# Kernel optimization log

Measured on AMD Instinct MI355X. Metric: run time of the kernel, lower is better.

## Reference

```python
import jax, jax.numpy as jnp
import numpy as np

D_MODEL = 1024
NUM_HEADS = 16
DEPTH = D_MODEL // NUM_HEADS  # 64
BATCH = 2
SEQ = 2048


def setup_inputs() -> dict:
    key = jax.random.key(0)
    ks = jax.random.split(key, 11)
    s = 0.02
    return {
        "q": jax.random.normal(ks[0], (BATCH, SEQ, D_MODEL), dtype=jnp.float32),
        "k": jax.random.normal(ks[1], (BATCH, SEQ, D_MODEL), dtype=jnp.float32),
        "v": jax.random.normal(ks[2], (BATCH, SEQ, D_MODEL), dtype=jnp.float32),
        "wq": jax.random.normal(ks[3], (D_MODEL, D_MODEL), dtype=jnp.float32) * s,
        "bq": jnp.zeros((D_MODEL,), dtype=jnp.float32),
        "wk": jax.random.normal(ks[4], (D_MODEL, D_MODEL), dtype=jnp.float32) * s,
        "bk": jnp.zeros((D_MODEL,), dtype=jnp.float32),
        "wv": jax.random.normal(ks[5], (D_MODEL, D_MODEL), dtype=jnp.float32) * s,
        "bv": jnp.zeros((D_MODEL,), dtype=jnp.float32),
        "wo": jax.random.normal(ks[6], (D_MODEL, D_MODEL), dtype=jnp.float32) * s,
        "bo": jnp.zeros((D_MODEL,), dtype=jnp.float32),
    }


def reference(q, k, v, wq, bq, wk, bk, wv, bv, wo, bo):
    B = q.shape[0]
    # QKV projections, then split heads: (B, S, H, D)
    qh = (q @ wq + bq).reshape(B, -1, NUM_HEADS, DEPTH)
    kh = (k @ wk + bk).reshape(B, -1, NUM_HEADS, DEPTH)
    vh = (v @ wv + bv).reshape(B, -1, NUM_HEADS, DEPTH)

    inv_sqrt_dk = 1.0 / jnp.sqrt(jnp.float32(DEPTH))
    # scores: (B, Lq, Lk, H)
    scores = jnp.einsum('blhd,bjhd->bljh', qh, kh) * inv_sqrt_dk
    attn = jax.nn.softmax(scores, axis=2)
    # NOTE: original code divides by sqrt(dk) a SECOND time after softmax (faithful quirk)
    attn = attn * inv_sqrt_dk
    out = jnp.einsum('bljh,bjhe->blhe', attn, vh).reshape(B, -1, NUM_HEADS * DEPTH)
    return out @ wo + bo
```

## Files before the change

### kernel.cpp

```cpp
#include <hip/hip_runtime.h>
#include <math.h>

#define D_MODEL 1024
#define NHEADS 16
#define DH 64
#define BATCH 2
#define SEQ 2048
#define M_TOTAL (BATCH * SEQ)

typedef __attribute__((ext_vector_type(8))) short bf16x8;
typedef __attribute__((ext_vector_type(4))) float f32x4;
typedef __attribute__((ext_vector_type(16))) float f32x16;
typedef __attribute__((ext_vector_type(8))) unsigned short ushort8;
typedef unsigned short u16;
typedef unsigned int u32;

#define SCALE_Q 0.18033688f

static __device__ __forceinline__ u16 f2bf(float x) {
  unsigned int u = __float_as_uint(x);
  unsigned int r = (u + 0x7fffu + ((u >> 16) & 1u)) >> 16;
  return (u16)r;
}
static __device__ __forceinline__ u32 pk2bf(float a, float b) {
  return (u32)f2bf(a) | ((u32)f2bf(b) << 16);
}
static __device__ __forceinline__ u32 pkhu(float a, float b) {
  return __builtin_amdgcn_perm(__float_as_uint(b) + 0x8000u,
                               __float_as_uint(a) + 0x8000u, 0x07060302u);
}
static __device__ __forceinline__ float exp2fast(float x) {
  return __builtin_amdgcn_exp2f(x);
}

static __device__ __forceinline__ void gl_lds16(const u16* g, u16* l) {
  __builtin_amdgcn_global_load_lds(
      (const __attribute__((address_space(1))) u32*)g,
      (__attribute__((address_space(3))) u32*)l, 16, 0, 0);
}

__global__ __launch_bounds__(256) void prep_kernel(
    const float* __restrict__ q, const float* __restrict__ k, const float* __restrict__ v,
    u16* __restrict__ qb, u16* __restrict__ kb, u16* __restrict__ vb,
    const float* __restrict__ w0, const float* __restrict__ w1,
    const float* __restrict__ w2, const float* __restrict__ w3,
    u16* __restrict__ t0, u16* __restrict__ t1,
    u16* __restrict__ t2, u16* __restrict__ t3) {
  __shared__ float tf[64 * 68];
  const int z = blockIdx.z;
  const int tid = threadIdx.x;
  if (z < 3) {
    const float* src = (z == 0) ? q : (z == 1) ? k : v;
    u16* dst = (z == 0) ? qb : (z == 1) ? kb : vb;
    const size_t i = ((size_t)blockIdx.x * 256 + tid) * 8;
    float4 a = *reinterpret_cast<const float4*>(src + i);
    float4 b = *reinterpret_cast<const float4*>(src + i + 4);
    u32 o0 = pk2bf(a.x, a.y), o1 = pk2bf(a.z, a.w);
    u32 o2 = pk2bf(b.x, b.y), o3 = pk2bf(b.z, b.w);
    *reinterpret_cast<uint4*>(dst + i) = make_uint4(o0, o1, o2, o3);
    return;
  }
  if (blockIdx.x >= 256) return;
  const int zz = z - 3;
  const float* w = (zz == 0) ? w0 : (zz == 1) ? w1 : (zz == 2) ? w2 : w3;
  u16* wt = (zz == 0) ? t0 : (zz == 1) ? t1 : (zz == 2) ? t2 : t3;
  const int n0 = (blockIdx.x & 15) * 64, k0 = (blockIdx.x >> 4) * 64;
  const int kl = tid >> 4, nq = (tid & 15) * 4;
#pragma unroll
  for (int c = 0; c < 4; ++c) {
    float4 vv = *reinterpret_cast<const float4*>(
        &w[(size_t)(k0 + kl + c * 16) * 1024 + n0 + nq]);
    *reinterpret_cast<float4*>(&tf[(kl + c * 16) * 68 + nq]) = vv;
  }
  __syncthreads();
  const int n = tid & 63, kq = tid >> 6;
  u32 pk[8];
#pragma unroll
  for (int p = 0; p < 8; ++p) {
    float a = tf[(kq * 16 + 2 * p) * 68 + n];
    float b = tf[(kq * 16 + 2 * p + 1) * 68 + n];
    pk[p] = pk2bf(a, b);
  }
  u16* dst = &wt[(size_t)(n0 + n) * 1024 + k0 + kq * 16];
  *reinterpret_cast<uint4*>(dst) = make_uint4(pk[0], pk[1], pk[2], pk[3]);
  *reinterpret_cast<uint4*>(dst + 8) = make_uint4(pk[4], pk[5], pk[6], pk[7]);
}

__global__ __launch_bounds__(256) void qkv_gemm_kernel(
    const u16* __restrict__ qb, const u16* __restrict__ kb, const u16* __restrict__ vb,
    const u16* __restrict__ wqT, const u16* __restrict__ wkT, const u16* __restrict__ wvT,
    const float* __restrict__ bq, const float* __restrict__ bk, const float* __restrict__ bv,
    u16* __restrict__ qh, u16* __restrict__ kh, u16* __restrict__ vhT) {
  __shared__ u16 lds[16384];

  const int z = blockIdx.z;
  const u16* A  = (z == 0) ? qb : (z == 1) ? kb : vb;
  const u16* BT = (z == 0) ? wqT : (z == 1) ? wkT : wvT;
  const float* bias = (z == 0) ? bq : (z == 1) ? bk : bv;

  int wg = blockIdx.x + 8 * blockIdx.y;
  wg = (wg & 7) * 32 + (wg >> 3);
  const int m0 = (wg >> 3) * 128;
  const int n0 = (wg & 7) * 128;

  const int tid = threadIdx.x;
  const int w = tid >> 6, l = tid & 63;
  const int wr = w >> 1, wc = w & 1;
  const int n = l & 15, g = l >> 4;

  const u16* Ab = A + (size_t)(m0 + w * 16 + (l >> 2)) * 1024 + (l & 3) * 8;
  const u16* Bb = BT + (size_t)(n0 + w * 16 + (l >> 2)) * 1024 + (l & 3) * 8;
  const int wb = w * 512;

  f32x4 acc[4][4];
#pragma unroll
  for (int fm = 0; fm < 4; ++fm)
#pragma unroll
    for (int fn = 0; fn < 4; ++fn) acc[fm][fn] = (f32x4)(0.0f);

  gl_lds16(Ab, lds + wb);
  gl_lds16(Ab + (size_t)64 * 1024, lds + wb + 2048);
  gl_lds16(Bb, lds + 8192 + wb);
  gl_lds16(Bb + (size_t)64 * 1024, lds + 8192 + wb + 2048);
  __syncthreads();

  int cur = 0;
  for (int kk = 0; kk < 1024; kk += 32) {
    u16* sAc = lds + cur * 4096;
    u16* sBc = lds + 8192 + cur * 4096;
    if (kk + 32 < 1024) {
      u16* sAn = lds + (cur ^ 1) * 4096;
      u16* sBn = lds + 8192 + (cur ^ 1) * 4096;
      gl_lds16(Ab + kk + 32, sAn + wb);
      gl_lds16(Ab + kk + 32 + (size_t)64 * 1024, sAn + wb + 2048);
      gl_lds16(Bb + kk + 32, sBn + wb);
      gl_lds16(Bb + kk + 32 + (size_t)64 * 1024, sBn + wb + 2048);
    }
    bf16x8 af[4], bf[4];
#pragma unroll
    for (int f = 0; f < 4; ++f)
      af[f] = *reinterpret_cast<const bf16x8*>(&sAc[(wr * 64 + f * 16 + n) * 32 + g * 8]);
#pragma unroll
    for (int f = 0; f < 4; ++f)
      bf[f] = *reinterpret_cast<const bf16x8*>(&sBc[(wc * 64 + f * 16 + n) * 32 + g * 8]);
#pragma unroll
    for (int fm = 0; fm < 4; ++fm)
#pragma unroll
      for (int fn = 0; fn < 4; ++fn)
        acc[fm][fn] = __builtin_amdgcn_mfma_f32_16x16x32_bf16(af[fm], bf[fn], acc[fm][fn], 0, 0, 0);
    __syncthreads();
    cur ^= 1;
  }

  float bv4[4];
#pragma unroll
  for (int fn = 0; fn < 4; ++fn) bv4[fn] = bias[n0 + wc * 64 + fn * 16 + n];

  if (z < 2) {
    const float scale = (z == 0) ? SCALE_Q : 1.0f;
    u16* dst = (z == 0) ? qh : kh;
#pragma unroll
    for (int fm = 0; fm < 4; ++fm)
#pragma unroll
      for (int fn = 0; fn < 4; ++fn)
#pragma unroll
        for (int rr = 0; rr < 4; ++rr) {
          const int row = m0 + wr * 64 + fm * 16 + g * 4 + rr;
          const int col = n0 + wc * 64 + fn * 16 + n;
          dst[(size_t)row * 1024 + col] = f2bf((acc[fm][fn][rr] + bv4[fn]) * scale);
        }
  } else {
    __syncthreads();
    u16* bw = lds + w * 2304;
    const int hh = (n0 >> 6) + wc;
    const int bb = m0 >> 11;
    const int c = l >> 1, half = l & 1;
    const int sbase = (m0 & 2047) + wr * 64 + half * 32;
#pragma unroll
    for (int p = 0; p < 2; ++p) {
#pragma unroll
      for (int fh = 0; fh < 2; ++fh) {
        const int fn = p * 2 + fh;
#pragma unroll
        for (int fm = 0; fm < 4; ++fm)
#pragma unroll
          for (int rr = 0; rr < 4; ++rr)
            bw[(fh * 16 + n) * 72 + fm * 16 + g * 4 + rr] =
                f2bf(acc[fm][fn][rr] + bv4[fn]);
      }
      __syncthreads();
      u16* gd = vhT + ((size_t)((bb * NHEADS + hh) * DH + p * 32 + c)) * SEQ + sbase;
#pragma unroll
      for (int j = 0; j < 4; ++j)
        *reinterpret_cast<uint4*>(gd + j * 8) =
            *reinterpret_cast<const uint4*>(&bw[c * 72 + half * 32 + j * 8]);
      __syncthreads();
    }
  }
}

__global__ __launch_bounds__(256) void out_gemm_kernel(
    const u16* __restrict__ aob, const u16* __restrict__ woT,
    const float* __restrict__ bo, float* __restrict__ out) {
  __shared__ u16 lds[12288];

  int wg = blockIdx.x + 16 * blockIdx.y;
  wg = (wg & 7) * 64 + (wg >> 3);
  const int m0 = (wg >> 4) * 128;
  const int n0 = (wg & 15) * 64;

  const int tid = threadIdx.x;
  const int w = tid >> 6, l = tid & 63;
  const int wr = w >> 1, wc = w & 1;
  const int n = l & 15, g = l >> 4;

  const u16* Ab = aob + (size_t)(m0 + w * 16 + (l >> 2)) * 1024 + (l & 3) * 8;
  const u16* Bb = woT + (size_t)(n0 + w * 16 + (l >> 2)) * 1024 + (l & 3) * 8;
  const int wb = w * 512;

  f32x4 acc[4][2];
#pragma unroll
  for (int fm = 0; fm < 4; ++fm)
#pragma unroll
    for (int fn = 0; fn < 2; ++fn) acc[fm][fn] = (f32x4)(0.0f);

  gl_lds16(Ab, lds + wb);
  gl_lds16(Ab + (size_t)64 * 1024, lds + wb + 2048);
  gl_lds16(Bb, lds + 8192 + wb);
  __syncthreads();

  int cur = 0;
  for (int kk = 0; kk < 1024; kk += 32) {
    u16* sAc = lds + cur * 4096;
    u16* sBc = lds + 8192 + cur * 2048;
    if (kk + 32 < 1024) {
      u16* sAn = lds + (cur ^ 1) * 4096;
      u16* sBn = lds + 8192 + (cur ^ 1) * 2048;
      gl_lds16(Ab + kk + 32, sAn + wb);
      gl_lds16(Ab + kk + 32 + (size_t)64 * 1024, sAn + wb + 2048);
      gl_lds16(Bb + kk + 32, sBn + wb);
    }
    bf16x8 af[4], bf[2];
#pragma unroll
    for (int f = 0; f < 4; ++f)
      af[f] = *reinterpret_cast<const bf16x8*>(&sAc[(wr * 64 + f * 16 + n) * 32 + g * 8]);
#pragma unroll
    for (int f = 0; f < 2; ++f)
      bf[f] = *reinterpret_cast<const bf16x8*>(&sBc[(wc * 32 + f * 16 + n) * 32 + g * 8]);
#pragma unroll
    for (int fm = 0; fm < 4; ++fm)
#pragma unroll
      for (int fn = 0; fn < 2; ++fn)
        acc[fm][fn] = __builtin_amdgcn_mfma_f32_16x16x32_bf16(af[fm], bf[fn], acc[fm][fn], 0, 0, 0);
    __syncthreads();
    cur ^= 1;
  }

  const float b0 = bo[n0 + wc * 32 + n];
  const float b1 = bo[n0 + wc * 32 + 16 + n];
#pragma unroll
  for (int fm = 0; fm < 4; ++fm)
#pragma unroll
    for (int rr = 0; rr < 4; ++rr) {
      const int row = m0 + wr * 64 + fm * 16 + g * 4 + rr;
      out[(size_t)row * 1024 + n0 + wc * 32 + n] = acc[fm][0][rr] + b0;
      out[(size_t)row * 1024 + n0 + wc * 32 + 16 + n] = acc[fm][1][rr] + b1;
    }
}

#define KT 64
__global__ __launch_bounds__(256, 2) void attn_mfma_kernel(
    const u16* __restrict__ qh, const u16* __restrict__ kh,
    const u16* __restrict__ vhT, u16* __restrict__ aob) {
  const int bid = blockIdx.x;
  const int xcd = bid & 7;
  const int idx = bid >> 3;
  const int bh = (xcd << 2) | (idx >> 4);
  const int qt = idx & 15;
  const int b = bh >> 4, h = bh & 15;

  const int tid = threadIdx.x;
  const int w = tid >> 6, l = tid & 63;
  const int lr = l & 31;
  const int g1 = l >> 5;
  const int q0 = qt * 128 + w * 32;

  __shared__ u16 Ks[2][KT * DH];
  __shared__ u16 Vs[2][DH * KT];

  union { u32 u[4]; bf16x8 v; } onesu;
  onesu.u[0] = onesu.u[1] = onesu.u[2] = onesu.u[3] = 0x3F803F80u;

  bf16x8 qf[4];
#pragma unroll
  for (int kq = 0; kq < 4; ++kq)
    qf[kq] = *reinterpret_cast<const bf16x8*>(
        &qh[((size_t)(b * SEQ + q0 + lr)) * D_MODEL + h * DH + kq * 16 + g1 * 8]);

  f32x16 O0 = (f32x16)(0.0f), O1 = (f32x16)(0.0f), L0 = (f32x16)(0.0f);

  const int srow = tid >> 2, sq = tid & 3;
  const u16* kp0 = kh + (size_t)(b * SEQ + srow) * D_MODEL + h * DH + sq * 16;
  const u16* vp0 = vhT + ((size_t)((b * NHEADS + h) * DH + srow)) * SEQ + sq * 16;
  const int sbase = srow * 64 + sq * 16;
  const int sxor = (srow & 7) << 3;
  const int rxor = (lr & 7) << 3;

  ushort8 kr[2], vr[2];
#pragma unroll
  for (int c = 0; c < 2; ++c) {
    kr[c] = *reinterpret_cast<const ushort8*>(kp0 + c * 8);
    vr[c] = *reinterpret_cast<const ushort8*>(vp0 + c * 8);
  }
#pragma unroll
  for (int c = 0; c < 2; ++c) {
    const int sidx = (sbase + c * 8) ^ sxor;
    *reinterpret_cast<ushort8*>(&Ks[0][sidx]) = kr[c];
    *reinterpret_cast<ushort8*>(&Vs[0][sidx]) = vr[c];
  }
  __syncthreads();

  int cur = 0;
  for (int jt = 0; jt < SEQ / KT; ++jt) {
    if (jt + 1 < SEQ / KT) {
      const int off = (jt + 1) * KT;
#pragma unroll
      for (int c = 0; c < 2; ++c) {
        kr[c] = *reinterpret_cast<const ushort8*>(kp0 + (size_t)off * D_MODEL + c * 8);
        vr[c] = *reinterpret_cast<const ushort8*>(vp0 + off + c * 8);
      }
    }

    __builtin_amdgcn_s_setprio(1);
    f32x16 St0 = (f32x16)(0.0f), St1 = (f32x16)(0.0f);
#pragma unroll
    for (int kq = 0; kq < 4; ++kq) {
      const int coff = kq * 16 + g1 * 8;
      bf16x8 kf0 = *reinterpret_cast<const bf16x8*>(&Ks[cur][(lr * 64 + coff) ^ rxor]);
      bf16x8 kf1 = *reinterpret_cast<const bf16x8*>(&Ks[cur][((32 + lr) * 64 + coff) ^ rxor]);
      St0 = __builtin_amdgcn_mfma_f32_32x32x16_bf16(kf0, qf[kq], St0, 0, 0, 0);
      St1 = __builtin_amdgcn_mfma_f32_32x32x16_bf16(kf1, qf[kq], St1, 0, 0, 0);
    }
    __builtin_amdgcn_s_setprio(0);

    u32 U0[8], U1[8];
#pragma unroll
    for (int s = 0; s < 8; ++s) {
      float a0 = exp2fast(St0[2 * s]), b0 = exp2fast(St0[2 * s + 1]);
      float a1 = exp2fast(St1[2 * s]), b1 = exp2fast(St1[2 * s + 1]);
      U0[s] = pkhu(a0, b0);
      U1[s] = pkhu(a1, b1);
    }

    __builtin_amdgcn_s_setprio(1);
#pragma unroll
    for (int kb2 = 0; kb2 < 2; ++kb2) {
#pragma unroll
      for (int m16 = 0; m16 < 2; ++m16) {
        union { u32 u[4]; bf16x8 v; } pa;
        if (kb2 == 0) {
          pa.u[0] = U0[m16 * 4 + 0]; pa.u[1] = U0[m16 * 4 + 1];
          pa.u[2] = U0[m16 * 4 + 2]; pa.u[3] = U0[m16 * 4 + 3];
        } else {
          pa.u[0] = U1[m16 * 4 + 0]; pa.u[1] = U1[m16 * 4 + 1];
          pa.u[2] = U1[m16 * 4 + 2]; pa.u[3] = U1[m16 * 4 + 3];
        }
        const int koff = kb2 * 32 + m16 * 16 + g1 * 4;
        union { u32 u[4]; bf16x8 v; } vb0, vb1;
        *reinterpret_cast<uint2*>(&vb0.u[0]) =
            *reinterpret_cast<const uint2*>(&Vs[cur][(lr * 64 + koff) ^ rxor]);
        *reinterpret_cast<uint2*>(&vb0.u[2]) =
            *reinterpret_cast<const uint2*>(&Vs[cur][(lr * 64 + koff + 8) ^ rxor]);
        *reinterpret_cast<uint2*>(&vb1.u[0]) =
            *reinterpret_cast<const uint2*>(&Vs[cur][((32 + lr) * 64 + koff) ^ rxor]);
        *reinterpret_cast<uint2*>(&vb1.u[2]) =
            *reinterpret_cast<const uint2*>(&Vs[cur][((32 + lr) * 64 + koff + 8) ^ rxor]);
        O0 = __builtin_amdgcn_mfma_f32_32x32x16_bf16(pa.v, vb0.v, O0, 0, 0, 0);
        O1 = __builtin_amdgcn_mfma_f32_32x32x16_bf16(pa.v, vb1.v, O1, 0, 0, 0);
        L0 = __builtin_amdgcn_mfma_f32_32x32x16_bf16(pa.v, onesu.v, L0, 0, 0, 0);
      }
    }
    __builtin_amdgcn_s_setprio(0);

    if (jt + 1 < SEQ / KT) {
#pragma unroll
      for (int c = 0; c < 2; ++c) {
        const int sidx = (sbase + c * 8) ^ sxor;
        *reinterpret_cast<ushort8*>(&Ks[cur ^ 1][sidx]) = kr[c];
        *reinterpret_cast<ushort8*>(&Vs[cur ^ 1][sidx]) = vr[c];
      }
    }
    __syncthreads();
    cur ^= 1;
  }

  float invr[16];
#pragma unroll
  for (int r = 0; r < 16; ++r) invr[r] = 0.125f / L0[r];
#pragma unroll
  for (int dblk = 0; dblk < 2; ++dblk) {
#pragma unroll
    for (int s = 0; s < 8; ++s) {
      const int r0 = 2 * s, r1 = 2 * s + 1;
      float x0 = (dblk ? O1[r0] : O0[r0]) * invr[r0];
      float x1 = (dblk ? O1[r1] : O0[r1]) * invr[r1];
      const int row0 = q0 + (r0 & 3) + 8 * (r0 >> 2) + 4 * g1;
      const int row1 = q0 + (r1 & 3) + 8 * (r1 >> 2) + 4 * g1;
      const int col = h * DH + dblk * 32 + lr;
      aob[((size_t)(b * SEQ + row0)) * D_MODEL + col] = f2bf(x0);
      aob[((size_t)(b * SEQ + row1)) * D_MODEL + col] = f2bf(x1);
    }
  }
}

extern "C" void kernel_launch(void* const* d_in, const int* in_sizes, int n_in,
                              void* d_out, int out_size, void* d_ws, size_t ws_size,
                              hipStream_t stream) {
  const float* q  = (const float*)d_in[0];
  const float* k  = (const float*)d_in[1];
  const float* v  = (const float*)d_in[2];
  const float* wq = (const float*)d_in[3];
  const float* bq = (const float*)d_in[4];
  const float* wk = (const float*)d_in[5];
  const float* bk = (const float*)d_in[6];
  const float* wv = (const float*)d_in[7];
  const float* bv = (const float*)d_in[8];
  const float* wo = (const float*)d_in[9];
  const float* bo = (const float*)d_in[10];
  float* out = (float*)d_out;

  const size_t wcount = (size_t)D_MODEL * D_MODEL;
  const size_t tcount = (size_t)M_TOTAL * D_MODEL;
  u16* wqT = (u16*)d_ws;
  u16* wkT = wqT + wcount;
  u16* wvT = wkT + wcount;
  u16* woT = wvT + wcount;
  u16* qb  = woT + wcount;
  u16* kb  = qb + tcount;
  u16* vb  = kb + tcount;
  u16* qh  = vb + tcount;
  u16* kh  = qh + tcount;
  u16* vhT = kh + tcount;
  u16* aob = qb;

  dim3 blk(256);

  prep_kernel<<<dim3(2048, 1, 7), blk, 0, stream>>>(
      q, k, v, qb, kb, vb, wq, wk, wv, wo, wqT, wkT, wvT, woT);

  qkv_gemm_kernel<<<dim3(8, 32, 3), blk, 0, stream>>>(
      qb, kb, vb, wqT, wkT, wvT, bq, bk, bv, qh, kh, vhT);

  attn_mfma_kernel<<<dim3(512), blk, 0, stream>>>(qh, kh, vhT, aob);

  out_gemm_kernel<<<dim3(16, 32), blk, 0, stream>>>(aob, woT, bo, out);
}
```

Measured before the change: 118.9 us.

## Give each attention wave two query subtiles and sum softmax rows in registers

The attention kernel now runs 128-thread blocks. Each wave owns 64 query rows split into two 32-row subtiles, so every K and V fragment read from LDS feeds twice as many MFMAs. The extra ones-vector MFMA that computed the softmax denominator is gone. Each lane now sums its exponentials in scalar registers, combines the two half-waves with a shuffle, and passes the sums through a small LDS buffer to the output layout. In exchange, per-wave register pressure rises and there are half as many resident waves to hide latency. The row sums also now use unrounded fp32 exponentials instead of the bf16-rounded ones.

```diff
diff --git a/kernel.cpp b/kernel.cpp
--- a/kernel.cpp
+++ b/kernel.cpp
@@ -269,7 +269,7 @@
 }
 
 #define KT 64
-__global__ __launch_bounds__(256, 2) void attn_mfma_kernel(
+__global__ __launch_bounds__(128, 1) void attn_mfma_kernel(
     const u16* __restrict__ qh, const u16* __restrict__ kh,
     const u16* __restrict__ vhT, u16* __restrict__ aob) {
   const int bid = blockIdx.x;
@@ -283,37 +283,40 @@
   const int w = tid >> 6, l = tid & 63;
   const int lr = l & 31;
   const int g1 = l >> 5;
-  const int q0 = qt * 128 + w * 32;
+  const int q0 = qt * 128 + w * 64;
 
   __shared__ u16 Ks[2][KT * DH];
   __shared__ u16 Vs[2][DH * KT];
-
-  union { u32 u[4]; bf16x8 v; } onesu;
-  onesu.u[0] = onesu.u[1] = onesu.u[2] = onesu.u[3] = 0x3F803F80u;
-
-  bf16x8 qf[4];
-#pragma unroll
-  for (int kq = 0; kq < 4; ++kq)
-    qf[kq] = *reinterpret_cast<const bf16x8*>(
+  __shared__ float Ls[2][2][32];
+
+  bf16x8 qfA[4], qfB[4];
+#pragma unroll
+  for (int kq = 0; kq < 4; ++kq) {
+    qfA[kq] = *reinterpret_cast<const bf16x8*>(
         &qh[((size_t)(b * SEQ + q0 + lr)) * D_MODEL + h * DH + kq * 16 + g1 * 8]);
-
-  f32x16 O0 = (f32x16)(0.0f), O1 = (f32x16)(0.0f), L0 = (f32x16)(0.0f);
-
-  const int srow = tid >> 2, sq = tid & 3;
-  const u16* kp0 = kh + (size_t)(b * SEQ + srow) * D_MODEL + h * DH + sq * 16;
-  const u16* vp0 = vhT + ((size_t)((b * NHEADS + h) * DH + srow)) * SEQ + sq * 16;
-  const int sbase = srow * 64 + sq * 16;
+    qfB[kq] = *reinterpret_cast<const bf16x8*>(
+        &qh[((size_t)(b * SEQ + q0 + 32 + lr)) * D_MODEL + h * DH + kq * 16 + g1 * 8]);
+  }
+
+  f32x16 O0A = (f32x16)(0.0f), O1A = (f32x16)(0.0f);
+  f32x16 O0B = (f32x16)(0.0f), O1B = (f32x16)(0.0f);
+  float lsumA = 0.0f, lsumB = 0.0f;
+
+  const int srow = tid >> 1, shalf = tid & 1;
+  const u16* kp0 = kh + (size_t)(b * SEQ + srow) * D_MODEL + h * DH + shalf * 32;
+  const u16* vp0 = vhT + ((size_t)((b * NHEADS + h) * DH + srow)) * SEQ + shalf * 32;
+  const int sbase = srow * 64 + shalf * 32;
   const int sxor = (srow & 7) << 3;
   const int rxor = (lr & 7) << 3;
 
-  ushort8 kr[2], vr[2];
-#pragma unroll
-  for (int c = 0; c < 2; ++c) {
+  ushort8 kr[4], vr[4];
+#pragma unroll
+  for (int c = 0; c < 4; ++c) {
     kr[c] = *reinterpret_cast<const ushort8*>(kp0 + c * 8);
     vr[c] = *reinterpret_cast<const ushort8*>(vp0 + c * 8);
   }
 #pragma unroll
-  for (int c = 0; c < 2; ++c) {
+  for (int c = 0; c < 4; ++c) {
     const int sidx = (sbase + c * 8) ^ sxor;
     *reinterpret_cast<ushort8*>(&Ks[0][sidx]) = kr[c];
     *reinterpret_cast<ushort8*>(&Vs[0][sidx]) = vr[c];
@@ -325,31 +328,43 @@
     if (jt + 1 < SEQ / KT) {
       const int off = (jt + 1) * KT;
 #pragma unroll
-      for (int c = 0; c < 2; ++c) {
+      for (int c = 0; c < 4; ++c) {
         kr[c] = *reinterpret_cast<const ushort8*>(kp0 + (size_t)off * D_MODEL + c * 8);
         vr[c] = *reinterpret_cast<const ushort8*>(vp0 + off + c * 8);
       }
     }
 
     __builtin_amdgcn_s_setprio(1);
-    f32x16 St0 = (f32x16)(0.0f), St1 = (f32x16)(0.0f);
+    f32x16 StA0 = (f32x16)(0.0f), StA1 = (f32x16)(0.0f);
+    f32x16 StB0 = (f32x16)(0.0f), StB1 = (f32x16)(0.0f);
 #pragma unroll
     for (int kq = 0; kq < 4; ++kq) {
       const int coff = kq * 16 + g1 * 8;
       bf16x8 kf0 = *reinterpret_cast<const bf16x8*>(&Ks[cur][(lr * 64 + coff) ^ rxor]);
       bf16x8 kf1 = *reinterpret_cast<const bf16x8*>(&Ks[cur][((32 + lr) * 64 + coff) ^ rxor]);
-      St0 = __builtin_amdgcn_mfma_f32_32x32x16_bf16(kf0, qf[kq], St0, 0, 0, 0);
-      St1 = __builtin_amdgcn_mfma_f32_32x32x16_bf16(kf1, qf[kq], St1, 0, 0, 0);
+      StA0 = __builtin_amdgcn_mfma_f32_32x32x16_bf16(kf0, qfA[kq], StA0, 0, 0, 0);
+      StA1 = __builtin_amdgcn_mfma_f32_32x32x16_bf16(kf1, qfA[kq], StA1, 0, 0, 0);
+      StB0 = __builtin_amdgcn_mfma_f32_32x32x16_bf16(kf0, qfB[kq], StB0, 0, 0, 0);
+      StB1 = __builtin_amdgcn_mfma_f32_32x32x16_bf16(kf1, qfB[kq], StB1, 0, 0, 0);
     }
     __builtin_amdgcn_s_setprio(0);
 
-    u32 U0[8], U1[8];
+    u32 UA0[8], UA1[8], UB0[8], UB1[8];
 #pragma unroll
     for (int s = 0; s < 8; ++s) {
-      float a0 = exp2fast(St0[2 * s]), b0 = exp2fast(St0[2 * s + 1]);
-      float a1 = exp2fast(St1[2 * s]), b1 = exp2fast(St1[2 * s + 1]);
-      U0[s] = pkhu(a0, b0);
-      U1[s] = pkhu(a1, b1);
+      float a0 = exp2fast(StA0[2 * s]), b0 = exp2fast(StA0[2 * s + 1]);
+      float a1 = exp2fast(StA1[2 * s]), b1 = exp2fast(StA1[2 * s + 1]);
+      lsumA += (a0 + b0) + (a1 + b1);
+      UA0[s] = pkhu(a0, b0);
+      UA1[s] = pkhu(a1, b1);
+    }
+#pragma unroll
+    for (int s = 0; s < 8; ++s) {
+      float a0 = exp2fast(StB0[2 * s]), b0 = exp2fast(StB0[2 * s + 1]);
+      float a1 = exp2fast(StB1[2 * s]), b1 = exp2fast(StB1[2 * s + 1]);
+      lsumB += (a0 + b0) + (a1 + b1);
+      UB0[s] = pkhu(a0, b0);
+      UB1[s] = pkhu(a1, b1);
     }
 
     __builtin_amdgcn_s_setprio(1);
@@ -357,13 +372,17 @@
     for (int kb2 = 0; kb2 < 2; ++kb2) {
 #pragma unroll
       for (int m16 = 0; m16 < 2; ++m16) {
-        union { u32 u[4]; bf16x8 v; } pa;
+        union { u32 u[4]; bf16x8 v; } paA, paB;
         if (kb2 == 0) {
-          pa.u[0] = U0[m16 * 4 + 0]; pa.u[1] = U0[m16 * 4 + 1];
-          pa.u[2] = U0[m16 * 4 + 2]; pa.u[3] = U0[m16 * 4 + 3];
+          paA.u[0] = UA0[m16 * 4 + 0]; paA.u[1] = UA0[m16 * 4 + 1];
+          paA.u[2] = UA0[m16 * 4 + 2]; paA.u[3] = UA0[m16 * 4 + 3];
+          paB.u[0] = UB0[m16 * 4 + 0]; paB.u[1] = UB0[m16 * 4 + 1];
+          paB.u[2] = UB0[m16 * 4 + 2]; paB.u[3] = UB0[m16 * 4 + 3];
         } else {
-          pa.u[0] = U1[m16 * 4 + 0]; pa.u[1] = U1[m16 * 4 + 1];
-          pa.u[2] = U1[m16 * 4 + 2]; pa.u[3] = U1[m16 * 4 + 3];
+          paA.u[0] = UA1[m16 * 4 + 0]; paA.u[1] = UA1[m16 * 4 + 1];
+          paA.u[2] = UA1[m16 * 4 + 2]; paA.u[3] = UA1[m16 * 4 + 3];
+          paB.u[0] = UB1[m16 * 4 + 0]; paB.u[1] = UB1[m16 * 4 + 1];
+          paB.u[2] = UB1[m16 * 4 + 2]; paB.u[3] = UB1[m16 * 4 + 3];
         }
         const int koff = kb2 * 32 + m16 * 16 + g1 * 4;
         union { u32 u[4]; bf16x8 v; } vb0, vb1;
@@ -375,16 +394,17 @@
             *reinterpret_cast<const uint2*>(&Vs[cur][((32 + lr) * 64 + koff) ^ rxor]);
         *reinterpret_cast<uint2*>(&vb1.u[2]) =
             *reinterpret_cast<const uint2*>(&Vs[cur][((32 + lr) * 64 + koff + 8) ^ rxor]);
-        O0 = __builtin_amdgcn_mfma_f32_32x32x16_bf16(pa.v, vb0.v, O0, 0, 0, 0);
-        O1 = __builtin_amdgcn_mfma_f32_32x32x16_bf16(pa.v, vb1.v, O1, 0, 0, 0);
-        L0 = __builtin_amdgcn_mfma_f32_32x32x16_bf16(pa.v, onesu.v, L0, 0, 0, 0);
+        O0A = __builtin_amdgcn_mfma_f32_32x32x16_bf16(paA.v, vb0.v, O0A, 0, 0, 0);
+        O1A = __builtin_amdgcn_mfma_f32_32x32x16_bf16(paA.v, vb1.v, O1A, 0, 0, 0);
+        O0B = __builtin_amdgcn_mfma_f32_32x32x16_bf16(paB.v, vb0.v, O0B, 0, 0, 0);
+        O1B = __builtin_amdgcn_mfma_f32_32x32x16_bf16(paB.v, vb1.v, O1B, 0, 0, 0);
       }
     }
     __builtin_amdgcn_s_setprio(0);
 
     if (jt + 1 < SEQ / KT) {
 #pragma unroll
-      for (int c = 0; c < 2; ++c) {
+      for (int c = 0; c < 4; ++c) {
         const int sidx = (sbase + c * 8) ^ sxor;
         *reinterpret_cast<ushort8*>(&Ks[cur ^ 1][sidx]) = kr[c];
         *reinterpret_cast<ushort8*>(&Vs[cur ^ 1][sidx]) = vr[c];
@@ -394,21 +414,42 @@
     cur ^= 1;
   }
 
-  float invr[16];
-#pragma unroll
-  for (int r = 0; r < 16; ++r) invr[r] = 0.125f / L0[r];
-#pragma unroll
-  for (int dblk = 0; dblk < 2; ++dblk) {
-#pragma unroll
-    for (int s = 0; s < 8; ++s) {
-      const int r0 = 2 * s, r1 = 2 * s + 1;
-      float x0 = (dblk ? O1[r0] : O0[r0]) * invr[r0];
-      float x1 = (dblk ? O1[r1] : O0[r1]) * invr[r1];
-      const int row0 = q0 + (r0 & 3) + 8 * (r0 >> 2) + 4 * g1;
-      const int row1 = q0 + (r1 & 3) + 8 * (r1 >> 2) + 4 * g1;
-      const int col = h * DH + dblk * 32 + lr;
-      aob[((size_t)(b * SEQ + row0)) * D_MODEL + col] = f2bf(x0);
-      aob[((size_t)(b * SEQ + row1)) * D_MODEL + col] = f2bf(x1);
+  lsumA += (float)__shfl_xor(lsumA, 32);
+  lsumB += (float)__shfl_xor(lsumB, 32);
+  if (g1 == 0) {
+    Ls[w][0][lr] = lsumA;
+    Ls[w][1][lr] = lsumB;
+  }
+#pragma unroll
+  for (int ss = 0; ss < 2; ++ss) {
+    float invr[16];
+#pragma unroll
+    for (int c = 0; c < 4; ++c) {
+      float4 lv = *reinterpret_cast<const float4*>(&Ls[w][ss][c * 8 + g1 * 4]);
+      invr[c * 4 + 0] = 0.125f / lv.x;
+      invr[c * 4 + 1] = 0.125f / lv.y;
+      invr[c * 4 + 2] = 0.125f / lv.z;
+      invr[c * 4 + 3] = 0.125f / lv.w;
+    }
+#pragma unroll
+    for (int dblk = 0; dblk < 2; ++dblk) {
+#pragma unroll
+      for (int s = 0; s < 8; ++s) {
+        const int r0 = 2 * s, r1 = 2 * s + 1;
+        float x0, x1;
+        if (ss == 0) {
+          x0 = (dblk ? O1A[r0] : O0A[r0]) * invr[r0];
+          x1 = (dblk ? O1A[r1] : O0A[r1]) * invr[r1];
+        } else {
+          x0 = (dblk ? O1B[r0] : O0B[r0]) * invr[r0];
+          x1 = (dblk ? O1B[r1] : O0B[r1]) * invr[r1];
+        }
+        const int row0 = q0 + ss * 32 + (r0 & 3) + 8 * (r0 >> 2) + 4 * g1;
+        const int row1 = q0 + ss * 32 + (r1 & 3) + 8 * (r1 >> 2) + 4 * g1;
+        const int col = h * DH + dblk * 32 + lr;
+        aob[((size_t)(b * SEQ + row0)) * D_MODEL + col] = f2bf(x0);
+        aob[((size_t)(b * SEQ + row1)) * D_MODEL + col] = f2bf(x1);
+      }
     }
   }
 }
@@ -451,7 +492,7 @@
   qkv_gemm_kernel<<<dim3(8, 32, 3), blk, 0, stream>>>(
       qb, kb, vb, wqT, wkT, wvT, bq, bk, bv, qh, kh, vhT);
 
-  attn_mfma_kernel<<<dim3(512), blk, 0, stream>>>(qh, kh, vhT, aob);
+  attn_mfma_kernel<<<dim3(512), dim3(128), 0, stream>>>(qh, kh, vhT, aob);
 
   out_gemm_kernel<<<dim3(16, 32), blk, 0, stream>>>(aob, woT, bo, out);
 }
```

Result: slower. 131.3 us (+10.4%).

## Fuse fp32-to-bf16 activation conversion into QKV GEMM A-tile loads

Applied to the files above, without the earlier changes.

The separate pass that converted q/k/v activations to bf16 in the prep kernel is removed. The QKV GEMM now loads fp32 A tiles into registers, converts them to bf16, and writes them to LDS after the MFMAs, so they stay double-buffered. This drops a full read and write of three activation tensors. In exchange the GEMM reads twice as many A bytes from global memory, and the A path moves from async global-to-LDS loads to register staging, which raises register pressure.

```diff
diff --git a/kernel.cpp b/kernel.cpp
--- a/kernel.cpp
+++ b/kernel.cpp
@@ -40,8 +40,6 @@
 }
 
 __global__ __launch_bounds__(256) void prep_kernel(
-    const float* __restrict__ q, const float* __restrict__ k, const float* __restrict__ v,
-    u16* __restrict__ qb, u16* __restrict__ kb, u16* __restrict__ vb,
     const float* __restrict__ w0, const float* __restrict__ w1,
     const float* __restrict__ w2, const float* __restrict__ w3,
     u16* __restrict__ t0, u16* __restrict__ t1,
@@ -49,21 +47,8 @@
   __shared__ float tf[64 * 68];
   const int z = blockIdx.z;
   const int tid = threadIdx.x;
-  if (z < 3) {
-    const float* src = (z == 0) ? q : (z == 1) ? k : v;
-    u16* dst = (z == 0) ? qb : (z == 1) ? kb : vb;
-    const size_t i = ((size_t)blockIdx.x * 256 + tid) * 8;
-    float4 a = *reinterpret_cast<const float4*>(src + i);
-    float4 b = *reinterpret_cast<const float4*>(src + i + 4);
-    u32 o0 = pk2bf(a.x, a.y), o1 = pk2bf(a.z, a.w);
-    u32 o2 = pk2bf(b.x, b.y), o3 = pk2bf(b.z, b.w);
-    *reinterpret_cast<uint4*>(dst + i) = make_uint4(o0, o1, o2, o3);
-    return;
-  }
-  if (blockIdx.x >= 256) return;
-  const int zz = z - 3;
-  const float* w = (zz == 0) ? w0 : (zz == 1) ? w1 : (zz == 2) ? w2 : w3;
-  u16* wt = (zz == 0) ? t0 : (zz == 1) ? t1 : (zz == 2) ? t2 : t3;
+  const float* w = (z == 0) ? w0 : (z == 1) ? w1 : (z == 2) ? w2 : w3;
+  u16* wt = (z == 0) ? t0 : (z == 1) ? t1 : (z == 2) ? t2 : t3;
   const int n0 = (blockIdx.x & 15) * 64, k0 = (blockIdx.x >> 4) * 64;
   const int kl = tid >> 4, nq = (tid & 15) * 4;
 #pragma unroll
@@ -87,14 +72,14 @@
 }
 
 __global__ __launch_bounds__(256) void qkv_gemm_kernel(
-    const u16* __restrict__ qb, const u16* __restrict__ kb, const u16* __restrict__ vb,
+    const float* __restrict__ q, const float* __restrict__ k, const float* __restrict__ v,
     const u16* __restrict__ wqT, const u16* __restrict__ wkT, const u16* __restrict__ wvT,
     const float* __restrict__ bq, const float* __restrict__ bk, const float* __restrict__ bv,
     u16* __restrict__ qh, u16* __restrict__ kh, u16* __restrict__ vhT) {
   __shared__ u16 lds[16384];
 
   const int z = blockIdx.z;
-  const u16* A  = (z == 0) ? qb : (z == 1) ? kb : vb;
+  const float* A = (z == 0) ? q : (z == 1) ? k : v;
   const u16* BT = (z == 0) ? wqT : (z == 1) ? wkT : wvT;
   const float* bias = (z == 0) ? bq : (z == 1) ? bk : bv;
 
@@ -108,7 +93,9 @@
   const int wr = w >> 1, wc = w & 1;
   const int n = l & 15, g = l >> 4;
 
-  const u16* Ab = A + (size_t)(m0 + w * 16 + (l >> 2)) * 1024 + (l & 3) * 8;
+  const int arow = tid >> 1, ahalf = tid & 1;
+  const float* Ap = A + (size_t)(m0 + arow) * 1024 + ahalf * 16;
+  u16* sAw_base = lds + arow * 32 + ahalf * 16;
   const u16* Bb = BT + (size_t)(n0 + w * 16 + (l >> 2)) * 1024 + (l & 3) * 8;
   const int wb = w * 512;
 
@@ -118,24 +105,35 @@
 #pragma unroll
     for (int fn = 0; fn < 4; ++fn) acc[fm][fn] = (f32x4)(0.0f);
 
-  gl_lds16(Ab, lds + wb);
-  gl_lds16(Ab + (size_t)64 * 1024, lds + wb + 2048);
+  float4 a4[4];
+#pragma unroll
+  for (int c = 0; c < 4; ++c)
+    a4[c] = *reinterpret_cast<const float4*>(Ap + c * 4);
   gl_lds16(Bb, lds + 8192 + wb);
   gl_lds16(Bb + (size_t)64 * 1024, lds + 8192 + wb + 2048);
+  {
+    uint4 ua = make_uint4(pk2bf(a4[0].x, a4[0].y), pk2bf(a4[0].z, a4[0].w),
+                          pk2bf(a4[1].x, a4[1].y), pk2bf(a4[1].z, a4[1].w));
+    uint4 ub = make_uint4(pk2bf(a4[2].x, a4[2].y), pk2bf(a4[2].z, a4[2].w),
+                          pk2bf(a4[3].x, a4[3].y), pk2bf(a4[3].z, a4[3].w));
+    *reinterpret_cast<uint4*>(sAw_base) = ua;
+    *reinterpret_cast<uint4*>(sAw_base + 8) = ub;
+  }
   __syncthreads();
 
   int cur = 0;
   for (int kk = 0; kk < 1024; kk += 32) {
+    const bool has_next = (kk + 32 < 1024);
+    if (has_next) {
+#pragma unroll
+      for (int c = 0; c < 4; ++c)
+        a4[c] = *reinterpret_cast<const float4*>(Ap + kk + 32 + c * 4);
+      u16* sBn = lds + 8192 + (cur ^ 1) * 4096;
+      gl_lds16(Bb + kk + 32, sBn + wb);
+      gl_lds16(Bb + kk + 32 + (size_t)64 * 1024, sBn + wb + 2048);
+    }
     u16* sAc = lds + cur * 4096;
     u16* sBc = lds + 8192 + cur * 4096;
-    if (kk + 32 < 1024) {
-      u16* sAn = lds + (cur ^ 1) * 4096;
-      u16* sBn = lds + 8192 + (cur ^ 1) * 4096;
-      gl_lds16(Ab + kk + 32, sAn + wb);
-      gl_lds16(Ab + kk + 32 + (size_t)64 * 1024, sAn + wb + 2048);
-      gl_lds16(Bb + kk + 32, sBn + wb);
-      gl_lds16(Bb + kk + 32 + (size_t)64 * 1024, sBn + wb + 2048);
-    }
     bf16x8 af[4], bf[4];
 #pragma unroll
     for (int f = 0; f < 4; ++f)
@@ -148,6 +146,15 @@
 #pragma unroll
       for (int fn = 0; fn < 4; ++fn)
         acc[fm][fn] = __builtin_amdgcn_mfma_f32_16x16x32_bf16(af[fm], bf[fn], acc[fm][fn], 0, 0, 0);
+    if (has_next) {
+      u16* sAn = lds + (cur ^ 1) * 4096 + arow * 32 + ahalf * 16;
+      uint4 ua = make_uint4(pk2bf(a4[0].x, a4[0].y), pk2bf(a4[0].z, a4[0].w),
+                            pk2bf(a4[1].x, a4[1].y), pk2bf(a4[1].z, a4[1].w));
+      uint4 ub = make_uint4(pk2bf(a4[2].x, a4[2].y), pk2bf(a4[2].z, a4[2].w),
+                            pk2bf(a4[3].x, a4[3].y), pk2bf(a4[3].z, a4[3].w));
+      *reinterpret_cast<uint4*>(sAn) = ua;
+      *reinterpret_cast<uint4*>(sAn + 8) = ub;
+    }
     __syncthreads();
     cur ^= 1;
   }
@@ -435,21 +442,18 @@
   u16* wkT = wqT + wcount;
   u16* wvT = wkT + wcount;
   u16* woT = wvT + wcount;
-  u16* qb  = woT + wcount;
-  u16* kb  = qb + tcount;
-  u16* vb  = kb + tcount;
-  u16* qh  = vb + tcount;
+  u16* qh  = woT + wcount;
   u16* kh  = qh + tcount;
   u16* vhT = kh + tcount;
-  u16* aob = qb;
+  u16* aob = vhT + tcount;
 
   dim3 blk(256);
 
-  prep_kernel<<<dim3(2048, 1, 7), blk, 0, stream>>>(
-      q, k, v, qb, kb, vb, wq, wk, wv, wo, wqT, wkT, wvT, woT);
+  prep_kernel<<<dim3(256, 1, 4), blk, 0, stream>>>(
+      wq, wk, wv, wo, wqT, wkT, wvT, woT);
 
   qkv_gemm_kernel<<<dim3(8, 32, 3), blk, 0, stream>>>(
-      qb, kb, vb, wqT, wkT, wvT, bq, bk, bv, qh, kh, vhT);
+      q, k, v, wqT, wkT, wvT, bq, bk, bv, qh, kh, vhT);
 
   attn_mfma_kernel<<<dim3(512), blk, 0, stream>>>(qh, kh, vhT, aob);
 
```

Result: slower. 151.1 us (+27.0%).
